# Performance work log

Hardware: AMD Instinct MI355X
Metric: run time of the kernel (lower is better)

## Reference

```python
import jax, jax.numpy as jnp
import numpy as np

B = 16          # graphs per batch
T = 50          # cell types
C = 200         # neurons per cell type
N = T * C       # nodes per graph (10000)
NT = B * N      # total nodes (160000)
FEAT = 1        # num_node_features (forced to 1 by module structure)
H = 8           # attention heads
DEG = 32
E = NT * DEG    # edges (5.12M)
PASSES = 4
PERSIST = 1.0
EPS = 1e-5
TAU = 1.0
SLOPE = 0.2


def setup_inputs() -> dict:
    key = jax.random.key(0)
    ks = jax.random.split(key, 12)
    x = jax.random.normal(ks[0], (NT, FEAT), dtype=jnp.float32)
    # sprinkle exact zeros so the noise-injection branch is exercised
    x = jnp.where(jax.random.uniform(ks[1], x.shape) < 0.1, 0.0, x)
    # edges stay within each graph (batched disjoint graphs)
    dst = jax.random.randint(ks[2], (E,), 0, NT)
    src = (dst // N) * N + jax.random.randint(ks[3], (E,), 0, N)
    edge_index = jnp.stack([src, dst]).astype(jnp.int32)
    batch = (jnp.arange(NT) // N).astype(jnp.int32)
    perm_weights = jax.random.normal(ks[4], (T, B, C, C), dtype=jnp.float32)
    decision_vec = (jax.random.uniform(ks[5], (N,)) < 0.2).astype(jnp.float32)
    gat_w = jax.random.normal(ks[6], (FEAT, H), dtype=jnp.float32)
    att_src = jax.random.normal(ks[7], (H,), dtype=jnp.float32)
    att_dst = jax.random.normal(ks[8], (H,), dtype=jnp.float32)
    return {
        "x": x, "edge_index": edge_index, "batch": batch,
        "perm_weights": perm_weights, "decision_vec": decision_vec,
        "gat_w": gat_w, "att_src": att_src, "att_dst": att_dst,
        "gat_bias": jnp.zeros((1,), jnp.float32),
        "bn_gamma": jnp.ones((1,), jnp.float32),
        "bn_beta": jnp.zeros((1,), jnp.float32),
        "bn_mean": jnp.zeros((1,), jnp.float32),
        "bn_var": jnp.ones((1,), jnp.float32),
        "lin_w": jax.random.normal(ks[9], (1, 1), dtype=jnp.float32),
        "lin_b": jax.random.normal(ks[10], (1,), dtype=jnp.float32),
    }


def _permutation_layer(x, perm_weights, key):
    # x: [NT, FEAT] -> per-type blocks [T, B, C, FEAT]
    xb = x.reshape(B, T, C, FEAT).transpose(1, 0, 2, 3)
    u = jax.random.uniform(key, perm_weights.shape, minval=1e-10, maxval=1.0)
    gumbel = -jnp.log(-jnp.log(u))
    # F.gumbel_softmax(weights, dim=1) on [B,C,C] -> softmax over row axis (axis=2 here)
    soft = jax.nn.softmax((perm_weights + gumbel) / TAU, axis=2)
    y = jnp.einsum('tbij,tbjf->tbif', soft, xb)
    return y.transpose(1, 0, 2, 3).reshape(NT, FEAT)


def _add_noise(x, key):
    nz = x != 0
    n = nz.sum().astype(x.dtype)
    mean = jnp.sum(jnp.where(nz, x, 0.0)) / n
    var = jnp.sum(jnp.where(nz, (x - mean) ** 2, 0.0)) / (n - 1.0)  # unbiased, as torch .std()
    std = jnp.sqrt(var)
    noise = (std / 100.0) * jax.random.normal(key, x.shape, dtype=x.dtype)
    return jnp.where(nz, x, noise)


def _gat_conv(x, src, dst, gat_w, att_src, att_dst, gat_bias):
    xs = x @ gat_w                                   # [NT, H] (out_channels=1 per head)
    a_src = xs * att_src                             # [NT, H]
    a_dst = xs * att_dst
    e = a_src[src] + a_dst[dst]                      # [E+NT, H]
    e = jnp.where(e > 0, e, SLOPE * e)               # leaky_relu(0.2)
    emax = jax.ops.segment_max(e, dst, num_segments=NT)
    ee = jnp.exp(e - emax[dst])
    denom = jax.ops.segment_sum(ee, dst, num_segments=NT)
    alpha = ee / denom[dst]
    out = jax.ops.segment_sum(alpha * xs[src], dst, num_segments=NT)  # [NT, H]
    return out.mean(axis=1, keepdims=True) + gat_bias  # concat=False -> mean over heads


def reference(x, edge_index, batch, perm_weights, decision_vec, gat_w, att_src,
              att_dst, gat_bias, bn_gamma, bn_beta, bn_mean, bn_var, lin_w, lin_b):
    rk = jax.random.key(42)
    x = _permutation_layer(x, perm_weights, jax.random.fold_in(rk, 0))
    x_res = x
    x = _add_noise(x, jax.random.fold_in(rk, 1))
    # GATConv adds self loops by default
    loops = jnp.arange(NT, dtype=edge_index.dtype)
    src = jnp.concatenate([edge_index[0], loops])
    dst = jnp.concatenate([edge_index[1], loops])
    for i in range(PASSES):
        x = _gat_conv(x, src, dst, gat_w, att_src, att_dst, gat_bias)
        x = (x - bn_mean) / jnp.sqrt(bn_var + EPS) * bn_gamma + bn_beta  # eval BN
        x = jax.nn.silu(x)
        # dropout is identity in eval mode
        x = x + x_res * (PERSIST ** i)
    mask = jnp.tile(decision_vec, B)[:, None]        # [NT, 1]
    x = x * mask
    pooled = jax.ops.segment_max(x, batch, num_segments=B)  # global_max_pool -> [B, 1]
    return jax.nn.relu(pooled @ lin_w.T + lin_b)
```

## Files before the change

### kernel.cpp

```cpp
#include <hip/hip_runtime.h>
#include <stdint.h>
#include <math.h>

#define B_   16
#define T_   50
#define C_   200
#define N_   10000
#define NT_  160000
#define H_   8
#define E_   5120000
#define EPS_ 1e-5f
#define NB_  625
#define EB_  512
#define EPB_ 10000
#define ATH_ 1024
#define GB_  16
#define GC_  625
#define GTH_ 640
#define JC_  5
#define JW_  40
#define ROWP_ 41
#define LOG2E_ 1.44269504088896340736f

__device__ __forceinline__ float ex2(float x){
  float r; asm("v_exp_f32 %0, %1" : "=v"(r) : "v"(x)); return r;
}
__device__ __forceinline__ float lg2(float x){
  float r; asm("v_log_f32 %0, %1" : "=v"(r) : "v"(x)); return r;
}

__device__ __forceinline__ int wscan_incl(int v, int lane){
#pragma unroll
  for (int d = 1; d < 64; d <<= 1){
    int t = __shfl_up(v, d, 64);
    if (lane >= d) v += t;
  }
  return v;
}

struct TF2C { unsigned a, b; };
constexpr unsigned rotl32c(unsigned v, int r){ return (v << r) | (v >> (32 - r)); }
constexpr TF2C tf_const(unsigned k0, unsigned k1, unsigned x0, unsigned x1){
  unsigned ks2 = k0 ^ k1 ^ 0x1BD11BDAu;
  unsigned ks[3] = {k0, k1, ks2};
  x0 += k0; x1 += k1;
  const int RA[4] = {13, 15, 26, 6};
  const int RB[4] = {17, 29, 16, 24};
  for (int g = 0; g < 5; ++g){
    for (int r = 0; r < 4; ++r){
      int rr = (g & 1) ? RB[r] : RA[r];
      x0 += x1; x1 = rotl32c(x1, rr); x1 ^= x0;
    }
    x0 += ks[(g + 1) % 3];
    x1 += ks[(g + 2) % 3] + (unsigned)(g + 1);
  }
  return TF2C{x0, x1};
}
constexpr TF2C KG = tf_const(0u, 42u, 0u, 0u);
constexpr TF2C KN = tf_const(0u, 42u, 0u, 1u);

#define ROTL_(x, r) __builtin_amdgcn_alignbit((x), (x), 32 - (r))

__device__ __forceinline__ void tf2(unsigned k0, unsigned k1, unsigned x0, unsigned x1,
                                    unsigned &o0, unsigned &o1){
  unsigned ks2 = k0 ^ k1 ^ 0x1BD11BDAu;
  x0 += k0; x1 += k1;
#define TFR_(R) { x0 += x1; x1 = ROTL_(x1, R); x1 ^= x0; }
  TFR_(13) TFR_(15) TFR_(26) TFR_(6)  x0 += k1;  x1 += ks2 + 1u;
  TFR_(17) TFR_(29) TFR_(16) TFR_(24) x0 += ks2; x1 += k0 + 2u;
  TFR_(13) TFR_(15) TFR_(26) TFR_(6)  x0 += k0;  x1 += k1 + 3u;
  TFR_(17) TFR_(29) TFR_(16) TFR_(24) x0 += k1;  x1 += ks2 + 4u;
  TFR_(13) TFR_(15) TFR_(26) TFR_(6)  x0 += ks2; x1 += k0 + 5u;
#undef TFR_
  o0 = x0; o1 = x1;
}
__device__ __forceinline__ unsigned rbits(unsigned ka, unsigned kb, unsigned m){
  unsigned a, b; tf2(ka, kb, 0u, m, a, b); return a ^ b;
}

__device__ __forceinline__ float erfinv_xla(float x){
  float w = -log1pf(-x * x);
  float p;
  if (w < 5.0f){
    w = w - 2.5f;
    p = 2.81022636e-08f;
    p = fmaf(p, w, 3.43273939e-07f);
    p = fmaf(p, w, -3.5233877e-06f);
    p = fmaf(p, w, -4.39150654e-06f);
    p = fmaf(p, w, 0.00021858087f);
    p = fmaf(p, w, -0.00125372503f);
    p = fmaf(p, w, -0.00417768164f);
    p = fmaf(p, w, 0.246640727f);
    p = fmaf(p, w, 1.50140941f);
  } else {
    w = sqrtf(w) - 3.0f;
    p = -0.000200214257f;
    p = fmaf(p, w, 0.000100950558f);
    p = fmaf(p, w, 0.00134934322f);
    p = fmaf(p, w, -0.00367342844f);
    p = fmaf(p, w, 0.00573950773f);
    p = fmaf(p, w, -0.0076224613f);
    p = fmaf(p, w, 0.00943887047f);
    p = fmaf(p, w, 1.00167406f);
    p = fmaf(p, w, 2.83297682f);
  }
  return p * x;
}

__global__ __launch_bounds__(ATH_)
void k_hist(const int* __restrict__ dst, int* __restrict__ cnt){
  __shared__ int h[NB_];
  int tid = threadIdx.x, blk = blockIdx.x;
  for (int i = tid; i < NB_; i += ATH_) h[i] = 0;
  __syncthreads();
  int e0 = blk * EPB_;
  for (int i = tid; i < EPB_; i += ATH_)
    atomicAdd(&h[dst[e0 + i] >> 8], 1);
  __syncthreads();
  for (int i = tid; i < NB_; i += ATH_) cnt[blk * NB_ + i] = h[i];
}

__global__ __launch_bounds__(512)
void k_sumb(const int* __restrict__ cnt, int* __restrict__ bsum){
  __shared__ int sred[8];
  int b = blockIdx.x, tid = threadIdx.x;
  int v = cnt[tid * NB_ + b];
#pragma unroll
  for (int s = 32; s >= 1; s >>= 1) v += __shfl_xor(v, s, 64);
  int w = tid >> 6, l = tid & 63;
  if (l == 0) sred[w] = v;
  __syncthreads();
  if (tid == 0){
    int t = 0;
#pragma unroll
    for (int i = 0; i < 8; ++i) t += sred[i];
    bsum[b] = t;
  }
}

__global__ __launch_bounds__(640)
void k_scanb(const int* __restrict__ bsum, int* __restrict__ boff){
  __shared__ int wsum[16];
  int tid = threadIdx.x, lane = tid & 63, wid = tid >> 6;
  int v = (tid < NB_) ? bsum[tid] : 0;
  int inc = wscan_incl(v, lane);
  if (lane == 63) wsum[wid] = inc;
  __syncthreads();
  if (wid == 0){
    int wv = (lane < 10) ? wsum[lane] : 0;
    int wi = wscan_incl(wv, lane);
    if (lane < 10) wsum[lane] = wi - wv;
  }
  __syncthreads();
  if (tid < NB_) boff[tid] = inc - v + wsum[wid];
  if (tid == 0) boff[NB_] = E_;
}

__global__ __launch_bounds__(512)
void k_scanc(const int* __restrict__ cnt, const int* __restrict__ boff,
             int* __restrict__ gscan){
  __shared__ int wsum[8];
  int b = blockIdx.x, tid = threadIdx.x, lane = tid & 63, wid = tid >> 6;
  int v = cnt[tid * NB_ + b];
  int inc = wscan_incl(v, lane);
  if (lane == 63) wsum[wid] = inc;
  __syncthreads();
  int wp = 0;
#pragma unroll
  for (int k = 0; k < 8; ++k) wp += (k < wid) ? wsum[k] : 0;
  gscan[tid * NB_ + b] = boff[b] + inc - v + wp;
}

__global__ __launch_bounds__(ATH_)
void k_append(const int* __restrict__ src, const int* __restrict__ dst,
              const int* __restrict__ cnt, const int* __restrict__ gscan,
              unsigned* __restrict__ ebuf){
  __shared__ unsigned esh[EPB_];
  __shared__ int loff[NB_ + 1];
  __shared__ int cur[NB_];
  __shared__ int wsum[16];
  int tid = threadIdx.x, blk = blockIdx.x;
  int lane = tid & 63, wid = tid >> 6;
  int e0 = blk * EPB_;
  for (int i = tid; i < NB_; i += ATH_) cur[i] = 0;
  int hv = (tid < NB_) ? cnt[blk * NB_ + tid] : 0;
  int inc = wscan_incl(hv, lane);
  if (lane == 63 && wid < 10) wsum[wid] = inc;
  __syncthreads();
  if (wid == 0){
    int wv = (lane < 10) ? wsum[lane] : 0;
    int wi = wscan_incl(wv, lane);
    if (lane < 10) wsum[lane] = wi - wv;
  }
  __syncthreads();
  if (tid < NB_) loff[tid] = inc - hv + wsum[wid];
  if (tid == 0) loff[NB_] = EPB_;
  __syncthreads();
  for (int i = tid; i < EPB_; i += ATH_){
    int e = e0 + i;
    int d = dst[e];
    int b = d >> 8;
    int p = loff[b] + atomicAdd(&cur[b], 1);
    esh[p] = ((unsigned)src[e] << 8) | (unsigned)(d & 255);
  }
  __syncthreads();
  for (int b = wid; b < NB_; b += ATH_ / 64){
    int lo = loff[b], len = loff[b + 1] - lo;
    int gb0 = gscan[blk * NB_ + b];
    for (int p = lane; p < len; p += 64)
      ebuf[gb0 + p] = esh[lo + p];
  }
}

__global__ __launch_bounds__(512)
void k_bcsr(const int* __restrict__ boff, const unsigned* __restrict__ ebuf,
            int* __restrict__ offs, unsigned short* __restrict__ srcs16){
  __shared__ int cnt[256];
  __shared__ int cur[256];
  __shared__ int wsum[4];
  int b = blockIdx.x, tid = threadIdx.x, lane = tid & 63, wid = tid >> 6;
  int e0 = boff[b], e1 = boff[b + 1];
  int base_node = b * 256;
  int offA = (base_node / N_) * N_;
  int boundary = offA + N_;
  if (tid < 256) cnt[tid] = 0;
  __syncthreads();
  for (int e = e0 + tid; e < e1; e += 512)
    atomicAdd(&cnt[ebuf[e] & 255u], 1);
  __syncthreads();
  int v = (tid < 256) ? cnt[tid] : 0;
  int inc = wscan_incl(v, lane);
  if (lane == 63 && wid < 4) wsum[wid] = inc;
  __syncthreads();
  int wp = 0;
#pragma unroll
  for (int k = 0; k < 4; ++k) wp += (k < wid) ? wsum[k] : 0;
  int excl = inc - v + wp;
  if (tid < 256){ offs[base_node + tid] = e0 + excl; cur[tid] = excl; }
  __syncthreads();
  for (int e = e0 + tid; e < e1; e += 512){
    unsigned pk = ebuf[e];
    int dl = (int)(pk & 255u);
    int goff = (base_node + dl >= boundary) ? boundary : offA;
    int pos = e0 + atomicAdd(&cur[dl], 1);
    srcs16[pos] = (unsigned short)((int)(pk >> 8) - goff);
  }
  if (b == 0 && tid == 0) offs[NT_] = E_;
}

__global__ __launch_bounds__(512, 8)
void k_perm(const float* __restrict__ W, const float* __restrict__ x,
            float* __restrict__ ypart){
  __shared__ float ez[C_ * ROWP_];
  __shared__ float Ssh[JW_];
  __shared__ float rs[JW_];

  const int bid = blockIdx.x;
  const int tb = bid / JC_;
  const int jc = bid - tb * JC_;
  const int t = tb / B_;
  const int b = tb - t * B_;
  const int j0 = jc * JW_;
  const int xoff = (b * T_ + t) * C_;
  const int tid = threadIdx.x;
  const int w = tid >> 6, l = tid & 63;

  {
    int i = tid / JW_;
    int jj = tid - i * JW_;
    unsigned m = (unsigned)(tb * (C_ * C_) + i * C_ + j0 + jj);
    int la = i * ROWP_ + jj;
    int niter = (C_ * JW_ - tid + 511) >> 9;
    for (int it = 0; it < niter; ++it){
      unsigned bits = rbits(KG.a, KG.b, m);
      float fc = (float)(bits >> 9);
      float tneg;
      if (bits >= 0xFC000000u){
        float d = fmaf(-fc, 0x1p-23f, 1.0f);
        float p = 0.16666667f;
        p = fmaf(p, d, 0.2f);
        p = fmaf(p, d, 0.25f);
        p = fmaf(p, d, 0.33333333f);
        p = fmaf(p, d, 0.5f);
        p = fmaf(p, d, 1.0f);
        tneg = d * p;
      } else {
        float u = fmaf(fc, 0x1p-23f, 1e-10f);
        tneg = lg2(u) * -0.69314718056f;
      }
      ez[la] = ex2(W[m] * LOG2E_) * __builtin_amdgcn_rcpf(tneg);
      jj += 32;
      int wrap = jj >= JW_;
      jj = wrap ? jj - JW_ : jj;
      m += wrap ? 2592u : 2432u;
      la += wrap ? 525 : 524;
    }
  }
  __syncthreads();

#pragma unroll
  for (int q = 0; q < 5; ++q){
    int jj = w * 5 + q;
    float s = ez[l * ROWP_ + jj] + ez[(l + 64) * ROWP_ + jj] + ez[(l + 128) * ROWP_ + jj]
            + ((l < 8) ? ez[(l + 192) * ROWP_ + jj] : 0.f);
#pragma unroll
    for (int sh = 32; sh >= 1; sh >>= 1) s += __shfl_xor(s, sh, 64);
    if (l == 0) Ssh[jj] = s;
  }
  __syncthreads();
  if (tid < JW_) rs[tid] = x[xoff + j0 + tid] / Ssh[tid];
  __syncthreads();

  if (tid < C_){
    float acc = 0.f;
#pragma unroll 8
    for (int jj = 0; jj < JW_; ++jj)
      acc = fmaf(ez[tid * ROWP_ + jj], rs[jj], acc);
    ypart[jc * NT_ + xoff + tid] = acc;
  }
}

__global__ __launch_bounds__(256)
void k_ycomb(const float* __restrict__ ypart, float* __restrict__ y,
             float* __restrict__ spart){
  __shared__ float sred[12];
  int n = blockIdx.x * 256 + threadIdx.x;
  float v = 0.f;
#pragma unroll
  for (int jc = 0; jc < JC_; ++jc) v += ypart[jc * NT_ + n];
  y[n] = v;
  float s = 0.f, c = 0.f, q = 0.f;
  if (v != 0.f){ s = v; c = 1.f; q = v * v; }
#pragma unroll
  for (int sh = 32; sh >= 1; sh >>= 1){
    s += __shfl_xor(s, sh, 64);
    c += __shfl_xor(c, sh, 64);
    q += __shfl_xor(q, sh, 64);
  }
  int w = threadIdx.x >> 6, l = threadIdx.x & 63;
  if (l == 0){ sred[w] = s; sred[4 + w] = c; sred[8 + w] = q; }
  __syncthreads();
  if (threadIdx.x == 0){
    spart[blockIdx.x * 3 + 0] = sred[0] + sred[1] + sred[2] + sred[3];
    spart[blockIdx.x * 3 + 1] = sred[4] + sred[5] + sred[6] + sred[7];
    spart[blockIdx.x * 3 + 2] = sred[8] + sred[9] + sred[10] + sred[11];
  }
}

__global__ void k_stat2(const float* __restrict__ spart, float* __restrict__ stats){
  __shared__ float sred[12];
  int tid = threadIdx.x;
  float s = 0.f, c = 0.f, q = 0.f;
  for (int i = tid; i < 625; i += 256){
    s += spart[i * 3 + 0];
    c += spart[i * 3 + 1];
    q += spart[i * 3 + 2];
  }
#pragma unroll
  for (int sh = 32; sh >= 1; sh >>= 1){
    s += __shfl_xor(s, sh, 64);
    c += __shfl_xor(c, sh, 64);
    q += __shfl_xor(q, sh, 64);
  }
  int w = tid >> 6, l = tid & 63;
  if (l == 0){ sred[w] = s; sred[4 + w] = c; sred[8 + w] = q; }
  __syncthreads();
  if (tid == 0){
    float S = sred[0] + sred[1] + sred[2] + sred[3];
    float C = sred[4] + sred[5] + sred[6] + sred[7];
    float Q = sred[8] + sred[9] + sred[10] + sred[11];
    float var = (Q - S * S / C) / (C - 1.f);
    stats[0] = sqrtf(var) * 0.01f;
  }
}

__global__ void k_noise(const float* __restrict__ y, const float* __restrict__ stats,
                        float* __restrict__ x0){
  int n = blockIdx.x * 256 + threadIdx.x;
  float v = y[n];
  if (v != 0.0f){ x0[n] = v; return; }
  float scale = stats[0];
  unsigned bits = rbits(KN.a, KN.b, (unsigned)n);
  float f = __uint_as_float((bits >> 9) | 0x3f800000u) - 1.0f;
  float u = f * 2.0f + (-0.99999994f);
  u = fmaxf(-0.99999994f, u);
  float nrm = 1.41421356237f * erfinv_xla(u);
  x0[n] = scale * nrm;
}

__global__ __launch_bounds__(GTH_)
void k_gat(const float* __restrict__ xin, const float* __restrict__ xres,
           const int* __restrict__ offs, const unsigned short* __restrict__ srcs16,
           const float* __restrict__ gw, const float* __restrict__ asrc,
           const float* __restrict__ adst, const float* __restrict__ gbias,
           const float* __restrict__ bng, const float* __restrict__ bnb,
           const float* __restrict__ bnm, const float* __restrict__ bnv,
           float* __restrict__ xout){
  __shared__ float xsh[N_];
  int g = blockIdx.x / GB_, c = blockIdx.x - g * GB_;
  int tid = threadIdx.x;
  const float4* xv = (const float4*)(xin + g * N_);
  for (int i = tid; i < N_ / 4; i += GTH_) ((float4*)xsh)[i] = xv[i];
  __syncthreads();
  if (tid >= GC_) return;

  int nl = c * GC_ + tid;
  int n = g * N_ + nl;
  float xn = xsh[nl];

  float cs[H_], cdxn[H_], wv[H_];
#pragma unroll
  for (int h = 0; h < H_; ++h){
    wv[h] = gw[h];
    cs[h] = wv[h] * asrc[h] * LOG2E_;
    cdxn[h] = wv[h] * adst[h] * xn * LOG2E_;
  }
  float mh[H_], den[H_], num[H_];
#pragma unroll
  for (int h = 0; h < H_; ++h){
    float v = cs[h] * xn + cdxn[h];
    v = fmaxf(v, 0.2f * v);
    mh[h] = v; den[h] = 1.f; num[h] = xn;
  }
  int e0 = offs[n], e1 = offs[n + 1];
  for (int e = e0; e < e1; ++e){
    float xs = xsh[srcs16[e]];
#pragma unroll
    for (int h = 0; h < H_; ++h){
      float v = fmaf(cs[h], xs, cdxn[h]);
      v = fmaxf(v, 0.2f * v);
      float d = v - mh[h];
      float ed = ex2(-fabsf(d));
      bool newmax = d > 0.f;
      float corr = newmax ? ed : 1.f;
      float p    = newmax ? 1.f : ed;
      mh[h] = newmax ? v : mh[h];
      den[h] = fmaf(den[h], corr, p);
      num[h] = fmaf(num[h], corr, p * xs);
    }
  }
  float o = 0.f;
#pragma unroll
  for (int h = 0; h < H_; ++h) o += wv[h] * num[h] * __builtin_amdgcn_rcpf(den[h]);
  o = o * 0.125f + gbias[0];
  o = (o - bnm[0]) / sqrtf(bnv[0] + EPS_) * bng[0] + bnb[0];
  o = o / (1.0f + __expf(-o));
  xout[n] = o + xres[n];
}

__global__ __launch_bounds__(GTH_)
void k_pool1(const float* __restrict__ xf, const float* __restrict__ dv,
             float* __restrict__ pmax){
  __shared__ float sred[10];
  int g = blockIdx.x / GB_, c = blockIdx.x - g * GB_;
  int tid = threadIdx.x;
  float m = -INFINITY;
  if (tid < GC_){
    int nl = c * GC_ + tid;
    m = xf[g * N_ + nl] * dv[nl];
  }
#pragma unroll
  for (int s = 32; s >= 1; s >>= 1) m = fmaxf(m, __shfl_xor(m, s, 64));
  int w = tid >> 6, l = tid & 63;
  if (l == 0) sred[w] = m;
  __syncthreads();
  if (tid == 0){
    float p = sred[0];
#pragma unroll
    for (int i = 1; i < 10; ++i) p = fmaxf(p, sred[i]);
    pmax[blockIdx.x] = p;
  }
}

__global__ void k_pool2(const float* __restrict__ pmax, const float* __restrict__ lw,
                        const float* __restrict__ lb, float* __restrict__ out){
  int b = blockIdx.x, l = threadIdx.x;
  float m = (l < GB_) ? pmax[b * GB_ + l] : -INFINITY;
#pragma unroll
  for (int s = 32; s >= 1; s >>= 1) m = fmaxf(m, __shfl_xor(m, s, 64));
  if (l == 0){
    float o = m * lw[0] + lb[0];
    out[b] = (o > 0.f) ? o : 0.f;
  }
}

extern "C" void kernel_launch(void* const* d_in, const int* in_sizes, int n_in,
                              void* d_out, int out_size, void* d_ws, size_t ws_size,
                              hipStream_t stream){
  const float* x     = (const float*)d_in[0];
  const int*   ei    = (const int*)d_in[1];
  const float* W     = (const float*)d_in[3];
  const float* dv    = (const float*)d_in[4];
  const float* gw    = (const float*)d_in[5];
  const float* asrc  = (const float*)d_in[6];
  const float* adst  = (const float*)d_in[7];
  const float* gbias = (const float*)d_in[8];
  const float* bng   = (const float*)d_in[9];
  const float* bnb   = (const float*)d_in[10];
  const float* bnm   = (const float*)d_in[11];
  const float* bnv   = (const float*)d_in[12];
  const float* lw    = (const float*)d_in[13];
  const float* lb    = (const float*)d_in[14];
  float* out = (float*)d_out;

  char* ws = (char*)d_ws;
  int*            offs   = (int*)           (ws + 0);
  unsigned short* srcs16 = (unsigned short*)(ws + 640256);
  int*            cnt    = (int*)           (ws + 10880256);
  int*            gscan  = (int*)           (ws + 12160256);
  unsigned*       ebuf   = (unsigned*)      (ws + 21120256);
  float*          ypart  = (float*)         (ws + 21120256);
  float*          y      = (float*)         (ws + 41600256);
  float*          x0     = (float*)         (ws + 42240256);
  float*          x1     = (float*)         (ws + 42880256);
  int*            bsum   = (int*)           (ws + 43520256);
  int*            boff   = (int*)           (ws + 43522816);
  float*          pmax   = (float*)         (ws + 43525376);
  float*          stats  = (float*)         (ws + 43527936);
  float*          spart  = (float*)         (ws + 43527968);
  if (ws_size < (size_t)43535500) return;

  const int* esrc = ei;
  const int* edst = ei + E_;

  k_hist  <<<EB_, ATH_, 0, stream>>>(edst, cnt);
  k_sumb  <<<NB_, 512, 0, stream>>>(cnt, bsum);
  k_scanb <<<1, 640, 0, stream>>>(bsum, boff);
  k_scanc <<<NB_, 512, 0, stream>>>(cnt, boff, gscan);
  k_append<<<EB_, ATH_, 0, stream>>>(esrc, edst, cnt, gscan, ebuf);
  k_bcsr  <<<NB_, 512, 0, stream>>>(boff, ebuf, offs, srcs16);
  k_perm  <<<T_ * B_ * JC_, 512, 0, stream>>>(W, x, ypart);
  k_ycomb <<<625, 256, 0, stream>>>(ypart, y, spart);
  k_stat2 <<<1, 256, 0, stream>>>(spart, stats);
  k_noise <<<625, 256, 0, stream>>>(y, stats, x0);
  k_gat<<<B_ * GB_, GTH_, 0, stream>>>(x0, y, offs, srcs16, gw, asrc, adst, gbias, bng, bnb, bnm, bnv, x1);
  k_gat<<<B_ * GB_, GTH_, 0, stream>>>(x1, y, offs, srcs16, gw, asrc, adst, gbias, bng, bnb, bnm, bnv, x0);
  k_gat<<<B_ * GB_, GTH_, 0, stream>>>(x0, y, offs, srcs16, gw, asrc, adst, gbias, bng, bnb, bnm, bnv, x1);
  k_gat<<<B_ * GB_, GTH_, 0, stream>>>(x1, y, offs, srcs16, gw, asrc, adst, gbias, bng, bnb, bnm, bnv, x0);
  k_pool1 <<<B_ * GB_, GTH_, 0, stream>>>(x0, dv, pmax);
  k_pool2 <<<B_, 64, 0, stream>>>(pmax, lw, lb, out);
}
```

Measured before the change: 309.3 us.

## Fuse noise and pooling into GAT, vectorize perm weights, stage edges in LDS

Noise injection now happens while the first GAT pass loads the graph into shared memory, and max-pooling is fused into the last GAT pass. This removes two kernel launches and their global round trips. k_perm now loads weights as float4 and evaluates both log branches without divergence. k_bcsr stages each bucket's edges in shared memory so ebuf is read from global memory only once. The cost is extra LDS use and redundant noise generation, since every one of the 16 blocks per graph regenerates noise for the full graph.

```diff
diff --git a/kernel.cpp b/kernel.cpp
--- a/kernel.cpp
+++ b/kernel.cpp
@@ -20,6 +20,7 @@
 #define JC_  5
 #define JW_  40
 #define ROWP_ 41
+#define BCAP_ 10240
 #define LOG2E_ 1.44269504088896340736f
 
 __device__ __forceinline__ float ex2(float x){
@@ -215,18 +216,29 @@
 __global__ __launch_bounds__(512)
 void k_bcsr(const int* __restrict__ boff, const unsigned* __restrict__ ebuf,
             int* __restrict__ offs, unsigned short* __restrict__ srcs16){
+  __shared__ unsigned esh[BCAP_];
   __shared__ int cnt[256];
   __shared__ int cur[256];
   __shared__ int wsum[4];
   int b = blockIdx.x, tid = threadIdx.x, lane = tid & 63, wid = tid >> 6;
   int e0 = boff[b], e1 = boff[b + 1];
+  int len = e1 - e0;
   int base_node = b * 256;
   int offA = (base_node / N_) * N_;
   int boundary = offA + N_;
+  bool staged = (len <= BCAP_);
   if (tid < 256) cnt[tid] = 0;
   __syncthreads();
-  for (int e = e0 + tid; e < e1; e += 512)
-    atomicAdd(&cnt[ebuf[e] & 255u], 1);
+  if (staged){
+    for (int e = tid; e < len; e += 512){
+      unsigned pk = ebuf[e0 + e];
+      esh[e] = pk;
+      atomicAdd(&cnt[pk & 255u], 1);
+    }
+  } else {
+    for (int e = tid; e < len; e += 512)
+      atomicAdd(&cnt[ebuf[e0 + e] & 255u], 1);
+  }
   __syncthreads();
   int v = (tid < 256) ? cnt[tid] : 0;
   int inc = wscan_incl(v, lane);
@@ -238,12 +250,22 @@
   int excl = inc - v + wp;
   if (tid < 256){ offs[base_node + tid] = e0 + excl; cur[tid] = excl; }
   __syncthreads();
-  for (int e = e0 + tid; e < e1; e += 512){
-    unsigned pk = ebuf[e];
-    int dl = (int)(pk & 255u);
-    int goff = (base_node + dl >= boundary) ? boundary : offA;
-    int pos = e0 + atomicAdd(&cur[dl], 1);
-    srcs16[pos] = (unsigned short)((int)(pk >> 8) - goff);
+  if (staged){
+    for (int e = tid; e < len; e += 512){
+      unsigned pk = esh[e];
+      int dl = (int)(pk & 255u);
+      int goff = (base_node + dl >= boundary) ? boundary : offA;
+      int pos = e0 + atomicAdd(&cur[dl], 1);
+      srcs16[pos] = (unsigned short)((int)(pk >> 8) - goff);
+    }
+  } else {
+    for (int e = tid; e < len; e += 512){
+      unsigned pk = ebuf[e0 + e];
+      int dl = (int)(pk & 255u);
+      int goff = (base_node + dl >= boundary) ? boundary : offA;
+      int pos = e0 + atomicAdd(&cur[dl], 1);
+      srcs16[pos] = (unsigned short)((int)(pk >> 8) - goff);
+    }
   }
   if (b == 0 && tid == 0) offs[NT_] = E_;
 }
@@ -266,34 +288,40 @@
   const int w = tid >> 6, l = tid & 63;
 
   {
-    int i = tid / JW_;
-    int jj = tid - i * JW_;
-    unsigned m = (unsigned)(tb * (C_ * C_) + i * C_ + j0 + jj);
-    int la = i * ROWP_ + jj;
-    int niter = (C_ * JW_ - tid + 511) >> 9;
+    int i  = tid / 10;
+    int jq = tid - i * 10;
+    unsigned m = (unsigned)(tb * (C_ * C_) + i * C_ + j0 + 4 * jq);
+    int la = i * ROWP_ + 4 * jq;
+    int niter = (2000 - tid + 511) >> 9;
     for (int it = 0; it < niter; ++it){
-      unsigned bits = rbits(KG.a, KG.b, m);
-      float fc = (float)(bits >> 9);
-      float tneg;
-      if (bits >= 0xFC000000u){
-        float d = fmaf(-fc, 0x1p-23f, 1.0f);
-        float p = 0.16666667f;
+      float4 w4 = *reinterpret_cast<const float4*>(W + m);
+      unsigned bb0 = rbits(KG.a, KG.b, m);
+      unsigned bb1 = rbits(KG.a, KG.b, m + 1u);
+      unsigned bb2 = rbits(KG.a, KG.b, m + 2u);
+      unsigned bb3 = rbits(KG.a, KG.b, m + 3u);
+      unsigned bbv[4] = {bb0, bb1, bb2, bb3};
+      float wvv[4] = {w4.x, w4.y, w4.z, w4.w};
+#pragma unroll
+      for (int k = 0; k < 4; ++k){
+        unsigned bits = bbv[k];
+        float fc = (float)(bits >> 9);
+        float u  = fmaf(fc, 0x1p-23f, 1e-10f);
+        float tl = lg2(u) * -0.69314718056f;
+        float d  = fmaf(-fc, 0x1p-23f, 1.0f);
+        float p  = 0.16666667f;
         p = fmaf(p, d, 0.2f);
         p = fmaf(p, d, 0.25f);
         p = fmaf(p, d, 0.33333333f);
         p = fmaf(p, d, 0.5f);
         p = fmaf(p, d, 1.0f);
-        tneg = d * p;
-      } else {
-        float u = fmaf(fc, 0x1p-23f, 1e-10f);
-        tneg = lg2(u) * -0.69314718056f;
+        float tneg = (bits >= 0xFC000000u) ? d * p : tl;
+        ez[la + k] = ex2(wvv[k] * LOG2E_) * __builtin_amdgcn_rcpf(tneg);
       }
-      ez[la] = ex2(W[m] * LOG2E_) * __builtin_amdgcn_rcpf(tneg);
-      jj += 32;
-      int wrap = jj >= JW_;
-      jj = wrap ? jj - JW_ : jj;
-      m += wrap ? 2592u : 2432u;
-      la += wrap ? 525 : 524;
+      jq += 2;
+      int wrap = jq >= 10;
+      jq = wrap ? jq - 10 : jq;
+      m  += wrap ? 10368u : 10208u;
+      la += wrap ? 2100 : 2099;
     }
   }
   __syncthreads();
@@ -374,20 +402,7 @@
   }
 }
 
-__global__ void k_noise(const float* __restrict__ y, const float* __restrict__ stats,
-                        float* __restrict__ x0){
-  int n = blockIdx.x * 256 + threadIdx.x;
-  float v = y[n];
-  if (v != 0.0f){ x0[n] = v; return; }
-  float scale = stats[0];
-  unsigned bits = rbits(KN.a, KN.b, (unsigned)n);
-  float f = __uint_as_float((bits >> 9) | 0x3f800000u) - 1.0f;
-  float u = f * 2.0f + (-0.99999994f);
-  u = fmaxf(-0.99999994f, u);
-  float nrm = 1.41421356237f * erfinv_xla(u);
-  x0[n] = scale * nrm;
-}
-
+template<int MODE>
 __global__ __launch_bounds__(GTH_)
 void k_gat(const float* __restrict__ xin, const float* __restrict__ xres,
            const int* __restrict__ offs, const unsigned short* __restrict__ srcs16,
@@ -395,16 +410,33 @@
            const float* __restrict__ adst, const float* __restrict__ gbias,
            const float* __restrict__ bng, const float* __restrict__ bnb,
            const float* __restrict__ bnm, const float* __restrict__ bnv,
-           float* __restrict__ xout){
+           const float* __restrict__ stats, const float* __restrict__ dv,
+           float* __restrict__ xout, float* __restrict__ pmax){
   __shared__ float xsh[N_];
+  __shared__ float sred[10];
   int g = blockIdx.x / GB_, c = blockIdx.x - g * GB_;
   int tid = threadIdx.x;
-  const float4* xv = (const float4*)(xin + g * N_);
-  for (int i = tid; i < N_ / 4; i += GTH_) ((float4*)xsh)[i] = xv[i];
-  __syncthreads();
-  if (tid >= GC_) return;
-
-  int nl = c * GC_ + tid;
+  if (MODE == 1){
+    float scale = stats[0];
+    for (int i = tid; i < N_; i += GTH_){
+      float v = xin[g * N_ + i];
+      if (v == 0.0f){
+        unsigned bits = rbits(KN.a, KN.b, (unsigned)(g * N_ + i));
+        float f = __uint_as_float((bits >> 9) | 0x3f800000u) - 1.0f;
+        float u = fmaf(f, 2.0f, -0.99999994f);
+        u = fmaxf(-0.99999994f, u);
+        v = scale * 1.41421356237f * erfinv_xla(u);
+      }
+      xsh[i] = v;
+    }
+  } else {
+    const float4* xv = (const float4*)(xin + g * N_);
+    for (int i = tid; i < N_ / 4; i += GTH_) ((float4*)xsh)[i] = xv[i];
+  }
+  __syncthreads();
+
+  bool act = tid < GC_;
+  int nl = c * GC_ + (act ? tid : 0);
   int n = g * N_ + nl;
   float xn = xsh[nl];
 
@@ -422,7 +454,7 @@
     v = fmaxf(v, 0.2f * v);
     mh[h] = v; den[h] = 1.f; num[h] = xn;
   }
-  int e0 = offs[n], e1 = offs[n + 1];
+  int e0 = offs[n], e1 = act ? offs[n + 1] : e0;
   for (int e = e0; e < e1; ++e){
     float xs = xsh[srcs16[e]];
 #pragma unroll
@@ -445,30 +477,23 @@
   o = o * 0.125f + gbias[0];
   o = (o - bnm[0]) / sqrtf(bnv[0] + EPS_) * bng[0] + bnb[0];
   o = o / (1.0f + __expf(-o));
-  xout[n] = o + xres[n];
-}
-
-__global__ __launch_bounds__(GTH_)
-void k_pool1(const float* __restrict__ xf, const float* __restrict__ dv,
-             float* __restrict__ pmax){
-  __shared__ float sred[10];
-  int g = blockIdx.x / GB_, c = blockIdx.x - g * GB_;
-  int tid = threadIdx.x;
-  float m = -INFINITY;
-  if (tid < GC_){
-    int nl = c * GC_ + tid;
-    m = xf[g * N_ + nl] * dv[nl];
-  }
-#pragma unroll
-  for (int s = 32; s >= 1; s >>= 1) m = fmaxf(m, __shfl_xor(m, s, 64));
-  int w = tid >> 6, l = tid & 63;
-  if (l == 0) sred[w] = m;
-  __syncthreads();
-  if (tid == 0){
-    float p = sred[0];
-#pragma unroll
-    for (int i = 1; i < 10; ++i) p = fmaxf(p, sred[i]);
-    pmax[blockIdx.x] = p;
+  float res = o + xres[n];
+
+  if (MODE == 2){
+    float m2 = act ? res * dv[nl] : -INFINITY;
+#pragma unroll
+    for (int s = 32; s >= 1; s >>= 1) m2 = fmaxf(m2, __shfl_xor(m2, s, 64));
+    int wv2 = tid >> 6, l2 = tid & 63;
+    if (l2 == 0) sred[wv2] = m2;
+    __syncthreads();
+    if (tid == 0){
+      float p = sred[0];
+#pragma unroll
+      for (int i2 = 1; i2 < 10; ++i2) p = fmaxf(p, sred[i2]);
+      pmax[blockIdx.x] = p;
+    }
+  } else {
+    if (act) xout[n] = res;
   }
 }
 
@@ -532,11 +557,9 @@
   k_perm  <<<T_ * B_ * JC_, 512, 0, stream>>>(W, x, ypart);
   k_ycomb <<<625, 256, 0, stream>>>(ypart, y, spart);
   k_stat2 <<<1, 256, 0, stream>>>(spart, stats);
-  k_noise <<<625, 256, 0, stream>>>(y, stats, x0);
-  k_gat<<<B_ * GB_, GTH_, 0, stream>>>(x0, y, offs, srcs16, gw, asrc, adst, gbias, bng, bnb, bnm, bnv, x1);
-  k_gat<<<B_ * GB_, GTH_, 0, stream>>>(x1, y, offs, srcs16, gw, asrc, adst, gbias, bng, bnb, bnm, bnv, x0);
-  k_gat<<<B_ * GB_, GTH_, 0, stream>>>(x0, y, offs, srcs16, gw, asrc, adst, gbias, bng, bnb, bnm, bnv, x1);
-  k_gat<<<B_ * GB_, GTH_, 0, stream>>>(x1, y, offs, srcs16, gw, asrc, adst, gbias, bng, bnb, bnm, bnv, x0);
-  k_pool1 <<<B_ * GB_, GTH_, 0, stream>>>(x0, dv, pmax);
+  k_gat<1><<<B_ * GB_, GTH_, 0, stream>>>(y,  y, offs, srcs16, gw, asrc, adst, gbias, bng, bnb, bnm, bnv, stats, dv, x1, pmax);
+  k_gat<0><<<B_ * GB_, GTH_, 0, stream>>>(x1, y, offs, srcs16, gw, asrc, adst, gbias, bng, bnb, bnm, bnv, stats, dv, x0, pmax);
+  k_gat<0><<<B_ * GB_, GTH_, 0, stream>>>(x0, y, offs, srcs16, gw, asrc, adst, gbias, bng, bnb, bnm, bnv, stats, dv, x1, pmax);
+  k_gat<2><<<B_ * GB_, GTH_, 0, stream>>>(x1, y, offs, srcs16, gw, asrc, adst, gbias, bng, bnb, bnm, bnv, stats, dv, x0, pmax);
   k_pool2 <<<B_, 64, 0, stream>>>(pmax, lw, lb, out);
 }
```

Result: faster. 300.0 us (-3.0%).
